# Optimization experiments

Hardware: AMD Instinct MI355X
Metric: run time of the kernel (lower is better)

Reference implementation:

```python
import jax, jax.numpy as jnp
import numpy as np


def setup_inputs() -> dict:
    key = jax.random.key(0)
    k1, k2, k3, k4, k5 = jax.random.split(key, 5)
    B, S, T = 512, 1024, 32
    emissions = jax.random.normal(k1, (B, S, T), dtype=jnp.float32)
    tags = jax.random.randint(k2, (B, S), 0, T, dtype=jnp.int64)
    mask = jnp.ones((B, S), dtype=jnp.float32)  # all positions valid; mask[:,0]==1 required
    transitions = jax.random.normal(k3, (T, T), dtype=jnp.float32)
    start_transitions = jax.random.normal(k4, (T,), dtype=jnp.float32)
    end_transitions = jax.random.normal(k5, (T,), dtype=jnp.float32)
    return {
        "emissions": emissions,
        "tags": tags,
        "mask": mask,
        "transitions": transitions,
        "start_transitions": start_transitions,
        "end_transitions": end_transitions,
    }


def _compute_score(emissions, tags, mask, transitions, start_transitions, end_transitions):
    # score of the gold path, fully vectorized over time
    # first step
    score = start_transitions[tags[:, 0]]
    score = score + jnp.take_along_axis(emissions[:, 0], tags[:, 0:1], axis=1)[:, 0]
    # steps 1..S-1
    emit = jnp.take_along_axis(emissions[:, 1:], tags[:, 1:, None], axis=2)[..., 0]  # [B,S-1]
    trans = transitions[tags[:, :-1], tags[:, 1:]]                                   # [B,S-1]
    score = score + ((emit + trans) * mask[:, 1:]).sum(axis=1)
    # end transition from the last valid tag
    last_idx = mask.sum(axis=1).astype(jnp.int32) - 1                                # [B]
    last_tags = jnp.take_along_axis(tags, last_idx[:, None].astype(tags.dtype), axis=1)[:, 0]
    score = score + end_transitions[last_tags]
    return score


def _compute_partition(emissions, mask, transitions, start_transitions, end_transitions):
    # forward algorithm: logsumexp scan over time
    alpha0 = start_transitions + emissions[:, 0]  # [B,T]

    def step(alpha, inp):
        e_i, m_i = inp  # e_i: [B,T], m_i: [B]
        # alpha[b,i] + transitions[i,j] + e_i[b,j] -> logsumexp over i
        scores = alpha[:, :, None] + transitions[None, :, :] + e_i[:, None, :]  # [B,T,T]
        next_alpha = jax.nn.logsumexp(scores, axis=1)                            # [B,T]
        m = m_i[:, None]
        alpha = next_alpha * m + alpha * (1.0 - m)
        return alpha, None

    xs = (jnp.swapaxes(emissions[:, 1:], 0, 1), jnp.swapaxes(mask[:, 1:], 0, 1))
    alpha, _ = jax.lax.scan(step, alpha0, xs)
    alpha = alpha + end_transitions
    return jax.nn.logsumexp(alpha, axis=1)  # [B]


def reference(emissions, tags, mask, transitions, start_transitions, end_transitions):
    score = _compute_score(emissions, tags, mask, transitions, start_transitions, end_transitions)
    partition = _compute_partition(emissions, mask, transitions, start_transitions, end_transitions)
    return -(score - partition).sum()
```

## Files before the change

kernel.cpp:

```cpp
#include <hip/hip_runtime.h>


typedef __attribute__((ext_vector_type(8)))  short    short8;
typedef __attribute__((ext_vector_type(16))) float    f32x16;
typedef __attribute__((ext_vector_type(4)))  unsigned uint4v;

#define S_N 1024
#define T_N 32
#define B_N 512
#define L_CH 64
#define C_CH 16
#define SCALE_MUL 0.0078125f
#define SCALE_LOG 4.852030263919617f

#define WS_FRAG_DW ((size_t)B_N * C_CH * 512)
#define WS_MSUM_OFF (WS_FRAG_DW)
#define WS_SCORE_OFF (WS_FRAG_DW + 512)
#define WS_NAPP_OFF (WS_FRAG_DW + 1024)

#if __has_builtin(__builtin_amdgcn_cvt_pk_bf16_f32)
typedef __attribute__((ext_vector_type(2))) __bf16 bf16x2;
__device__ __forceinline__ unsigned cvtpk(float lo, float hi) {
    return __builtin_bit_cast(unsigned, __builtin_amdgcn_cvt_pk_bf16_f32(lo, hi));
}
#else
__device__ __forceinline__ unsigned cvtpk(float lo, float hi) {
    const unsigned a = __float_as_uint(lo) + 0x8000u;
    const unsigned b = __float_as_uint(hi) + 0x8000u;
    return __builtin_amdgcn_perm(b, a, 0x07060302u);
}
#endif

__device__ __forceinline__ short8 mk8(const unsigned* a) {
    uint4v u = {a[0], a[1], a[2], a[3]};
    return __builtin_bit_cast(short8, u);
}
__device__ __forceinline__ float bflo(unsigned u) { return __uint_as_float(u << 16); }
__device__ __forceinline__ float bfhi(unsigned u) { return __uint_as_float(u & 0xFFFF0000u); }
__device__ __forceinline__ int PIx(int x) { return (x & ~12) | ((x & 4) << 1) | ((x & 8) >> 1); }

__global__ __launch_bounds__(256) void crf_chunk(
    const float* __restrict__ em, const int* __restrict__ tags,
    const float* __restrict__ mask, const float* __restrict__ trans,
    const float* __restrict__ startT, unsigned* __restrict__ wsf,
    float* __restrict__ wsflt)
{
    __shared__ unsigned elds[4][L_CH * 16];
    const int wib  = threadIdx.x >> 6;
    const int lane = threadIdx.x & 63;
    const int n    = lane & 31;
    const int h    = lane >> 5;
    const int wave = blockIdx.x * 4 + wib;
    const int b    = wave >> 4;
    const int c    = wave & (C_CH - 1);

    unsigned* my = elds[wib];
    const float* eb = em + ((size_t)b * S_N + c * L_CH) * T_N;

    #pragma unroll
    for (int i = 0; i < 16; ++i) {
        const int flat = i * 64 + lane;
        const int r = flat >> 4, m = flat & 15;
        const int base = ((m & 4) << 2) + ((m & 2) << 2) + ((m & 1) << 1) + ((m >> 3) << 2);
        const float2 v = *(const float2*)(eb + r * 32 + base);
        my[r * 16 + m] = cvtpk(__expf(v.x) * SCALE_MUL, __expf(v.y) * SCALE_MUL);
    }

    const int s0 = c * L_CH;
    const float mv_l = mask[b * S_N + s0 + lane];
    unsigned long long mbits = __ballot(mv_l != 0.0f);
    if (c == 0) mbits &= ~1ull;

    {
        const int s  = s0 + lane;
        const int tc = tags[b * S_N + s];
        int tp = __shfl_up(tc, 1, 64);
        float val;
        if (lane == 0) {
            if (c == 0) {
                val = startT[tc] + eb[tc];
            } else {
                tp = tags[b * S_N + s - 1];
                val = mv_l * (em[((size_t)b * S_N + s) * T_N + tc] + trans[tp * 32 + tc]);
            }
        } else {
            val = mv_l * (em[((size_t)b * S_N + s) * T_N + tc] + trans[tp * 32 + tc]);
        }
        float ms = mv_l;
        #pragma unroll
        for (int d = 32; d > 0; d >>= 1) {
            val += __shfl_xor(val, d, 64);
            ms  += __shfl_xor(ms,  d, 64);
        }
        if (lane == 0) {
            atomicAdd(&wsflt[WS_SCORE_OFF + b], val);
            atomicAdd(&wsflt[WS_MSUM_OFF + b], ms);
            wsflt[WS_NAPP_OFF + b * C_CH + c] = (float)__popcll(mbits);
        }
    }
    __syncthreads();

    const bool fwdDir = (c < 8);
    const f32x16 Zacc = {};

    unsigned A1[4], A2[4];
    #pragma unroll
    for (int j = 0; j < 4; ++j) {
        const int k1 = PIx(8 * h + 2 * j);
        const int k2 = PIx(16 + 8 * h + 2 * j);
        if (fwdDir) {
            A1[j] = cvtpk(__expf(trans[n * 32 + k1]), __expf(trans[n * 32 + k1 + 1]));
            A2[j] = cvtpk(__expf(trans[n * 32 + k2]), __expf(trans[n * 32 + k2 + 1]));
        } else {
            A1[j] = cvtpk(__expf(trans[k1 * 32 + n]), __expf(trans[(k1 + 1) * 32 + n]));
            A2[j] = cvtpk(__expf(trans[k2 * 32 + n]), __expf(trans[(k2 + 1) * 32 + n]));
        }
    }
    const short8 A1v = mk8(A1), A2v = mk8(A2);
    const bool clean = ((mbits | (c == 0 ? 1ull : 0ull)) == ~0ull);

    if (fwdDir) {
        f32x16 D;
        #pragma unroll
        for (int i = 0; i < 16; ++i) {
            const int row = (i & 3) + 8 * (i >> 2) + 4 * h;
            D[i] = (row == n) ? 1.0f : 0.0f;
        }
        #define STEP_FWD(r_) { \
            const uint4 su = *(const uint4*)(my + (r_) * 16 + h * 8); \
            const uint4 sv = *(const uint4*)(my + (r_) * 16 + h * 8 + 4); \
            unsigned S[8]; \
            S[0] = cvtpk(D[0]  * bflo(su.x), D[1]  * bfhi(su.x)); \
            S[1] = cvtpk(D[2]  * bflo(su.y), D[3]  * bfhi(su.y)); \
            S[2] = cvtpk(D[4]  * bflo(su.z), D[5]  * bfhi(su.z)); \
            S[3] = cvtpk(D[6]  * bflo(su.w), D[7]  * bfhi(su.w)); \
            S[4] = cvtpk(D[8]  * bflo(sv.x), D[9]  * bfhi(sv.x)); \
            S[5] = cvtpk(D[10] * bflo(sv.y), D[11] * bfhi(sv.y)); \
            S[6] = cvtpk(D[12] * bflo(sv.z), D[13] * bfhi(sv.z)); \
            S[7] = cvtpk(D[14] * bflo(sv.w), D[15] * bfhi(sv.w)); \
            f32x16 t_ = __builtin_amdgcn_mfma_f32_32x32x16_bf16(A1v, mk8(&S[0]), Zacc, 0, 0, 0); \
            D = __builtin_amdgcn_mfma_f32_32x32x16_bf16(A2v, mk8(&S[4]), t_, 0, 0, 0); \
        }
        if (clean) {
            #pragma unroll 4
            for (int r = 63; r >= 1; --r) STEP_FWD(r);
            if (c != 0) STEP_FWD(0);
        } else {
            for (int r = 63; r >= 0; --r)
                if ((mbits >> r) & 1ull) STEP_FWD(r);
        }
        unsigned* dst = wsf + ((size_t)(b * C_CH + c) * 64 + lane) * 8;
        ((uint4*)dst)[0] = make_uint4(cvtpk(D[0], D[1]),  cvtpk(D[2], D[3]),
                                      cvtpk(D[4], D[5]),  cvtpk(D[6], D[7]));
        ((uint4*)dst)[1] = make_uint4(cvtpk(D[8], D[9]),  cvtpk(D[10], D[11]),
                                      cvtpk(D[12], D[13]), cvtpk(D[14], D[15]));
    } else {
        unsigned S[8] = {0u, 0u, 0u, 0u, 0u, 0u, 0u, 0u};
        {
            const int pn = PIx(n);
            if (((pn >> 3) & 1) == h) {
                const int j = pn & 7;
                const unsigned val = 0x3F80u << (16 * (j & 1));
                if (n < 16) S[j >> 1] |= val; else S[4 + (j >> 1)] |= val;
            }
        }
        #define STEP_BWD(r_) { \
            f32x16 t_ = __builtin_amdgcn_mfma_f32_32x32x16_bf16(A1v, mk8(&S[0]), Zacc, 0, 0, 0); \
            t_ = __builtin_amdgcn_mfma_f32_32x32x16_bf16(A2v, mk8(&S[4]), t_, 0, 0, 0); \
            const uint4 su = *(const uint4*)(my + (r_) * 16 + h * 8); \
            const uint4 sv = *(const uint4*)(my + (r_) * 16 + h * 8 + 4); \
            S[0] = cvtpk(t_[0]  * bflo(su.x), t_[1]  * bfhi(su.x)); \
            S[1] = cvtpk(t_[2]  * bflo(su.y), t_[3]  * bfhi(su.y)); \
            S[2] = cvtpk(t_[4]  * bflo(su.z), t_[5]  * bfhi(su.z)); \
            S[3] = cvtpk(t_[6]  * bflo(su.w), t_[7]  * bfhi(su.w)); \
            S[4] = cvtpk(t_[8]  * bflo(sv.x), t_[9]  * bfhi(sv.x)); \
            S[5] = cvtpk(t_[10] * bflo(sv.y), t_[11] * bfhi(sv.y)); \
            S[6] = cvtpk(t_[12] * bflo(sv.z), t_[13] * bfhi(sv.z)); \
            S[7] = cvtpk(t_[14] * bflo(sv.w), t_[15] * bfhi(sv.w)); \
        }
        if (clean) {
            #pragma unroll 4
            for (int r = 0; r < 64; ++r) STEP_BWD(r);
        } else {
            for (int r = 0; r < 64; ++r)
                if ((mbits >> r) & 1ull) STEP_BWD(r);
        }
        unsigned* dst = wsf + ((size_t)(b * C_CH + c) * 64 + lane) * 8;
        ((uint4*)dst)[0] = make_uint4(S[0], S[1], S[2], S[3]);
        ((uint4*)dst)[1] = make_uint4(S[4], S[5], S[6], S[7]);
    }
}

__global__ __launch_bounds__(128) void crf_combine(
    const float* __restrict__ em, const int* __restrict__ tags,
    const float* __restrict__ startT, const float* __restrict__ endT,
    const unsigned* __restrict__ wsf, const float* __restrict__ wsflt,
    float* __restrict__ out)
{
    __shared__ float sm[68];
    const int lane = threadIdx.x & 63;
    const int w = threadIdx.x >> 6;
    const int n = lane & 31, h = lane >> 5;
    const int b = blockIdx.x;

    int idxA[8], idxB[8];
    #pragma unroll
    for (int j = 0; j < 8; ++j) {
        idxA[j] = PIx(8 * h + j);
        idxB[j] = PIx(16 + 8 * h + j);
    }

    float a0 = (w == 0) ? (startT[n] + em[(size_t)b * S_N * T_N + n]) : endT[n];
    float m = a0;
    #pragma unroll
    for (int d = 16; d > 0; d >>= 1) m = fmaxf(m, __shfl_xor(m, d, 32));
    float A = __expf(a0 - m);
    float Lacc = m;
    float ntot = 0.0f;

    const uint4* fb = (const uint4*)(wsf + (size_t)b * C_CH * 512);
    const int c0 = (w == 0) ? 0 : 15;
    const int dc = (w == 0) ? 1 : -1;
    uint4 q0 = fb[c0 * 128 + lane * 2];
    uint4 q1 = fb[c0 * 128 + lane * 2 + 1];

    for (int i = 0; i < 8; ++i) {
        const int c = c0 + i * dc;
        uint4 n0 = q0, n1 = q1;
        if (i + 1 < 8) {
            n0 = fb[(c + dc) * 128 + lane * 2];
            n1 = fb[(c + dc) * 128 + lane * 2 + 1];
        }
        ntot += wsflt[WS_NAPP_OFF + b * C_CH + c];

        float p0 = 0.f, p1 = 0.f, p2 = 0.f, p3 = 0.f;
        p0 = fmaf(__shfl(A, idxA[0], 32), bflo(q0.x), p0);
        p1 = fmaf(__shfl(A, idxA[1], 32), bfhi(q0.x), p1);
        p2 = fmaf(__shfl(A, idxA[2], 32), bflo(q0.y), p2);
        p3 = fmaf(__shfl(A, idxA[3], 32), bfhi(q0.y), p3);
        p0 = fmaf(__shfl(A, idxA[4], 32), bflo(q0.z), p0);
        p1 = fmaf(__shfl(A, idxA[5], 32), bfhi(q0.z), p1);
        p2 = fmaf(__shfl(A, idxA[6], 32), bflo(q0.w), p2);
        p3 = fmaf(__shfl(A, idxA[7], 32), bfhi(q0.w), p3);
        p0 = fmaf(__shfl(A, idxB[0], 32), bflo(q1.x), p0);
        p1 = fmaf(__shfl(A, idxB[1], 32), bfhi(q1.x), p1);
        p2 = fmaf(__shfl(A, idxB[2], 32), bflo(q1.y), p2);
        p3 = fmaf(__shfl(A, idxB[3], 32), bfhi(q1.y), p3);
        p0 = fmaf(__shfl(A, idxB[4], 32), bflo(q1.z), p0);
        p1 = fmaf(__shfl(A, idxB[5], 32), bfhi(q1.z), p1);
        p2 = fmaf(__shfl(A, idxB[6], 32), bflo(q1.w), p2);
        p3 = fmaf(__shfl(A, idxB[7], 32), bfhi(q1.w), p3);
        float part = (p0 + p1) + (p2 + p3);
        part += __shfl_xor(part, 32);

        float mm = part;
        #pragma unroll
        for (int d = 16; d > 0; d >>= 1) mm = fmaxf(mm, __shfl_xor(mm, d, 32));
        A = part / mm;
        Lacc += __logf(mm);
        q0 = n0; q1 = n1;
    }

    if (h == 0) sm[w * 32 + n] = A;
    if (lane == 0) { sm[64 + w] = Lacc; sm[66 + w] = ntot; }
    __syncthreads();

    if (threadIdx.x < 32) {
        float v = sm[threadIdx.x] * sm[32 + threadIdx.x];
        #pragma unroll
        for (int d = 16; d > 0; d >>= 1) v += __shfl_xor(v, d, 32);
        if (threadIdx.x == 0) {
            const float part = sm[64] + sm[65] + __logf(v) + (sm[66] + sm[67]) * SCALE_LOG;
            const int len = (int)(wsflt[WS_MSUM_OFF + b] + 0.5f);
            const int lt  = tags[b * S_N + len - 1];
            atomicAdd(out, part - endT[lt] - wsflt[WS_SCORE_OFF + b]);
        }
    }
}

extern "C" void kernel_launch(void* const* d_in, const int* in_sizes, int n_in,
                              void* d_out, int out_size, void* d_ws, size_t ws_size,
                              hipStream_t stream) {
    const float* em     = (const float*)d_in[0];
    const int*   tags   = (const int*)  d_in[1];
    const float* mask   = (const float*)d_in[2];
    const float* trans  = (const float*)d_in[3];
    const float* startT = (const float*)d_in[4];
    const float* endT   = (const float*)d_in[5];
    float* out = (float*)d_out;

    unsigned* wsf   = (unsigned*)d_ws;
    float*    wsflt = (float*)d_ws;

    hipMemsetAsync(out, 0, sizeof(float), stream);
    hipMemsetAsync((char*)d_ws + WS_MSUM_OFF * 4, 0, 4096, stream);

    hipLaunchKernelGGL(crf_chunk, dim3(2048), dim3(256), 0, stream,
                       em, tags, mask, trans, startT, wsf, wsflt);
    hipLaunchKernelGGL(crf_combine, dim3(512), dim3(128), 0, stream,
                       em, tags, startT, endT, wsf, wsflt, out);
}
```

Measured before the change: 178.3 us.

## Interleave four independent chunk chains per wave and drop backward direction

Each wave now processes four sequence chunks with interleaved MFMA recurrences, so the dependent matrix-product chains can hide each other's MFMA latency. All chunks use forward direction, which removes the backward path. Work per batch moves into one block with 64KB LDS, and the grid shrinks to 512 blocks. The combine kernel becomes one wave per batch doing all 16 chunks sequentially, with no shared-memory merge. Register pressure rises from the four accumulators, the grid is smaller, and the combine serial chain doubles in length.

```diff
diff --git a/kernel.cpp b/kernel.cpp
--- a/kernel.cpp
+++ b/kernel.cpp
@@ -39,169 +39,154 @@
 __device__ __forceinline__ float bfhi(unsigned u) { return __uint_as_float(u & 0xFFFF0000u); }
 __device__ __forceinline__ int PIx(int x) { return (x & ~12) | ((x & 4) << 1) | ((x & 8) >> 1); }
 
-__global__ __launch_bounds__(256) void crf_chunk(
+__global__ __launch_bounds__(256, 2) void crf_chunk(
     const float* __restrict__ em, const int* __restrict__ tags,
     const float* __restrict__ mask, const float* __restrict__ trans,
     const float* __restrict__ startT, unsigned* __restrict__ wsf,
     float* __restrict__ wsflt)
 {
-    __shared__ unsigned elds[4][L_CH * 16];
+    __shared__ unsigned elds[16384];
     const int wib  = threadIdx.x >> 6;
     const int lane = threadIdx.x & 63;
     const int n    = lane & 31;
     const int h    = lane >> 5;
-    const int wave = blockIdx.x * 4 + wib;
-    const int b    = wave >> 4;
-    const int c    = wave & (C_CH - 1);
-
-    unsigned* my = elds[wib];
-    const float* eb = em + ((size_t)b * S_N + c * L_CH) * T_N;
-
-    #pragma unroll
-    for (int i = 0; i < 16; ++i) {
-        const int flat = i * 64 + lane;
-        const int r = flat >> 4, m = flat & 15;
-        const int base = ((m & 4) << 2) + ((m & 2) << 2) + ((m & 1) << 1) + ((m >> 3) << 2);
-        const float2 v = *(const float2*)(eb + r * 32 + base);
-        my[r * 16 + m] = cvtpk(__expf(v.x) * SCALE_MUL, __expf(v.y) * SCALE_MUL);
-    }
-
-    const int s0 = c * L_CH;
-    const float mv_l = mask[b * S_N + s0 + lane];
-    unsigned long long mbits = __ballot(mv_l != 0.0f);
-    if (c == 0) mbits &= ~1ull;
-
+    const int b    = blockIdx.x;
+
+    #pragma unroll
+    for (int q = 0; q < 4; ++q) {
+        const float* eq = em + ((size_t)b * S_N + (4 * wib + q) * L_CH) * T_N;
+        unsigned* mq = elds + wib * 4096 + q * 1024;
+        #pragma unroll
+        for (int i = 0; i < 16; ++i) {
+            const int flat = i * 64 + lane;
+            const int r = flat >> 4, m = flat & 15;
+            const int base = ((m & 4) << 2) + ((m & 2) << 2) + ((m & 1) << 1) + ((m >> 3) << 2);
+            const float2 v = *(const float2*)(eq + r * 32 + base);
+            mq[r * 16 + m] = cvtpk(__expf(v.x) * SCALE_MUL, __expf(v.y) * SCALE_MUL);
+        }
+    }
+
+    unsigned long long mb_[4];
     {
-        const int s  = s0 + lane;
-        const int tc = tags[b * S_N + s];
-        int tp = __shfl_up(tc, 1, 64);
-        float val;
+        float vacc = 0.f, macc = 0.f;
+        #pragma unroll
+        for (int q = 0; q < 4; ++q) {
+            const int c = 4 * wib + q;
+            const int s = c * L_CH + lane;
+            const float mv = mask[b * S_N + s];
+            unsigned long long mb = __ballot(mv != 0.0f);
+            if (c == 0) mb &= ~1ull;
+            mb_[q] = mb;
+            const int tc = tags[b * S_N + s];
+            int tp = __shfl_up(tc, 1, 64);
+            float val;
+            if (lane == 0) {
+                if (c == 0) {
+                    val = startT[tc] + em[(size_t)b * S_N * T_N + tc];
+                } else {
+                    tp = tags[b * S_N + s - 1];
+                    val = mv * (em[((size_t)b * S_N + s) * T_N + tc] + trans[tp * 32 + tc]);
+                }
+            } else {
+                val = mv * (em[((size_t)b * S_N + s) * T_N + tc] + trans[tp * 32 + tc]);
+            }
+            vacc += val; macc += mv;
+            if (lane == 0) wsflt[WS_NAPP_OFF + b * C_CH + c] = (float)__popcll(mb);
+        }
+        #pragma unroll
+        for (int d = 32; d > 0; d >>= 1) {
+            vacc += __shfl_xor(vacc, d, 64);
+            macc += __shfl_xor(macc, d, 64);
+        }
         if (lane == 0) {
-            if (c == 0) {
-                val = startT[tc] + eb[tc];
-            } else {
-                tp = tags[b * S_N + s - 1];
-                val = mv_l * (em[((size_t)b * S_N + s) * T_N + tc] + trans[tp * 32 + tc]);
-            }
-        } else {
-            val = mv_l * (em[((size_t)b * S_N + s) * T_N + tc] + trans[tp * 32 + tc]);
-        }
-        float ms = mv_l;
-        #pragma unroll
-        for (int d = 32; d > 0; d >>= 1) {
-            val += __shfl_xor(val, d, 64);
-            ms  += __shfl_xor(ms,  d, 64);
-        }
-        if (lane == 0) {
-            atomicAdd(&wsflt[WS_SCORE_OFF + b], val);
-            atomicAdd(&wsflt[WS_MSUM_OFF + b], ms);
-            wsflt[WS_NAPP_OFF + b * C_CH + c] = (float)__popcll(mbits);
-        }
-    }
-    __syncthreads();
-
-    const bool fwdDir = (c < 8);
-    const f32x16 Zacc = {};
+            atomicAdd(&wsflt[WS_SCORE_OFF + b], vacc);
+            atomicAdd(&wsflt[WS_MSUM_OFF + b], macc);
+        }
+    }
 
     unsigned A1[4], A2[4];
     #pragma unroll
     for (int j = 0; j < 4; ++j) {
         const int k1 = PIx(8 * h + 2 * j);
         const int k2 = PIx(16 + 8 * h + 2 * j);
-        if (fwdDir) {
-            A1[j] = cvtpk(__expf(trans[n * 32 + k1]), __expf(trans[n * 32 + k1 + 1]));
-            A2[j] = cvtpk(__expf(trans[n * 32 + k2]), __expf(trans[n * 32 + k2 + 1]));
-        } else {
-            A1[j] = cvtpk(__expf(trans[k1 * 32 + n]), __expf(trans[(k1 + 1) * 32 + n]));
-            A2[j] = cvtpk(__expf(trans[k2 * 32 + n]), __expf(trans[(k2 + 1) * 32 + n]));
-        }
+        A1[j] = cvtpk(__expf(trans[n * 32 + k1]), __expf(trans[n * 32 + k1 + 1]));
+        A2[j] = cvtpk(__expf(trans[n * 32 + k2]), __expf(trans[n * 32 + k2 + 1]));
     }
     const short8 A1v = mk8(A1), A2v = mk8(A2);
-    const bool clean = ((mbits | (c == 0 ? 1ull : 0ull)) == ~0ull);
-
-    if (fwdDir) {
-        f32x16 D;
-        #pragma unroll
-        for (int i = 0; i < 16; ++i) {
-            const int row = (i & 3) + 8 * (i >> 2) + 4 * h;
-            D[i] = (row == n) ? 1.0f : 0.0f;
-        }
-        #define STEP_FWD(r_) { \
-            const uint4 su = *(const uint4*)(my + (r_) * 16 + h * 8); \
-            const uint4 sv = *(const uint4*)(my + (r_) * 16 + h * 8 + 4); \
-            unsigned S[8]; \
-            S[0] = cvtpk(D[0]  * bflo(su.x), D[1]  * bfhi(su.x)); \
-            S[1] = cvtpk(D[2]  * bflo(su.y), D[3]  * bfhi(su.y)); \
-            S[2] = cvtpk(D[4]  * bflo(su.z), D[5]  * bfhi(su.z)); \
-            S[3] = cvtpk(D[6]  * bflo(su.w), D[7]  * bfhi(su.w)); \
-            S[4] = cvtpk(D[8]  * bflo(sv.x), D[9]  * bfhi(sv.x)); \
-            S[5] = cvtpk(D[10] * bflo(sv.y), D[11] * bfhi(sv.y)); \
-            S[6] = cvtpk(D[12] * bflo(sv.z), D[13] * bfhi(sv.z)); \
-            S[7] = cvtpk(D[14] * bflo(sv.w), D[15] * bfhi(sv.w)); \
-            f32x16 t_ = __builtin_amdgcn_mfma_f32_32x32x16_bf16(A1v, mk8(&S[0]), Zacc, 0, 0, 0); \
-            D = __builtin_amdgcn_mfma_f32_32x32x16_bf16(A2v, mk8(&S[4]), t_, 0, 0, 0); \
-        }
-        if (clean) {
-            #pragma unroll 4
-            for (int r = 63; r >= 1; --r) STEP_FWD(r);
-            if (c != 0) STEP_FWD(0);
-        } else {
-            for (int r = 63; r >= 0; --r)
-                if ((mbits >> r) & 1ull) STEP_FWD(r);
-        }
-        unsigned* dst = wsf + ((size_t)(b * C_CH + c) * 64 + lane) * 8;
-        ((uint4*)dst)[0] = make_uint4(cvtpk(D[0], D[1]),  cvtpk(D[2], D[3]),
-                                      cvtpk(D[4], D[5]),  cvtpk(D[6], D[7]));
-        ((uint4*)dst)[1] = make_uint4(cvtpk(D[8], D[9]),  cvtpk(D[10], D[11]),
-                                      cvtpk(D[12], D[13]), cvtpk(D[14], D[15]));
+    const f32x16 Zacc = {};
+
+    f32x16 D0, D1, D2, D3;
+    #pragma unroll
+    for (int i = 0; i < 16; ++i) {
+        const int row = (i & 3) + 8 * (i >> 2) + 4 * h;
+        const float v = (row == n) ? 1.0f : 0.0f;
+        D0[i] = v; D1[i] = v; D2[i] = v; D3[i] = v;
+    }
+
+    const unsigned* m0 = elds + wib * 4096;
+    const unsigned* m1 = m0 + 1024;
+    const unsigned* m2 = m0 + 2048;
+    const unsigned* m3 = m0 + 3072;
+
+    #define STEP(D, mq, r_) { \
+        const uint4 su = *(const uint4*)((mq) + (r_) * 16 + h * 8); \
+        const uint4 sv = *(const uint4*)((mq) + (r_) * 16 + h * 8 + 4); \
+        unsigned S[8]; \
+        S[0] = cvtpk(D[0]  * bflo(su.x), D[1]  * bfhi(su.x)); \
+        S[1] = cvtpk(D[2]  * bflo(su.y), D[3]  * bfhi(su.y)); \
+        S[2] = cvtpk(D[4]  * bflo(su.z), D[5]  * bfhi(su.z)); \
+        S[3] = cvtpk(D[6]  * bflo(su.w), D[7]  * bfhi(su.w)); \
+        S[4] = cvtpk(D[8]  * bflo(sv.x), D[9]  * bfhi(sv.x)); \
+        S[5] = cvtpk(D[10] * bflo(sv.y), D[11] * bfhi(sv.y)); \
+        S[6] = cvtpk(D[12] * bflo(sv.z), D[13] * bfhi(sv.z)); \
+        S[7] = cvtpk(D[14] * bflo(sv.w), D[15] * bfhi(sv.w)); \
+        f32x16 t_ = __builtin_amdgcn_mfma_f32_32x32x16_bf16(A1v, mk8(&S[0]), Zacc, 0, 0, 0); \
+        D = __builtin_amdgcn_mfma_f32_32x32x16_bf16(A2v, mk8(&S[4]), t_, 0, 0, 0); \
+    }
+
+    const bool allclean =
+        ((mb_[0] | ((4 * wib) == 0 ? 1ull : 0ull)) == ~0ull) &&
+        (mb_[1] == ~0ull) && (mb_[2] == ~0ull) && (mb_[3] == ~0ull);
+
+    if (allclean) {
+        #pragma unroll 2
+        for (int r = L_CH - 1; r >= 1; --r) {
+            STEP(D0, m0, r); STEP(D1, m1, r); STEP(D2, m2, r); STEP(D3, m3, r);
+        }
+        if (mb_[0] & 1ull) STEP(D0, m0, 0);
+        if (mb_[1] & 1ull) STEP(D1, m1, 0);
+        if (mb_[2] & 1ull) STEP(D2, m2, 0);
+        if (mb_[3] & 1ull) STEP(D3, m3, 0);
     } else {
-        unsigned S[8] = {0u, 0u, 0u, 0u, 0u, 0u, 0u, 0u};
-        {
-            const int pn = PIx(n);
-            if (((pn >> 3) & 1) == h) {
-                const int j = pn & 7;
-                const unsigned val = 0x3F80u << (16 * (j & 1));
-                if (n < 16) S[j >> 1] |= val; else S[4 + (j >> 1)] |= val;
-            }
-        }
-        #define STEP_BWD(r_) { \
-            f32x16 t_ = __builtin_amdgcn_mfma_f32_32x32x16_bf16(A1v, mk8(&S[0]), Zacc, 0, 0, 0); \
-            t_ = __builtin_amdgcn_mfma_f32_32x32x16_bf16(A2v, mk8(&S[4]), t_, 0, 0, 0); \
-            const uint4 su = *(const uint4*)(my + (r_) * 16 + h * 8); \
-            const uint4 sv = *(const uint4*)(my + (r_) * 16 + h * 8 + 4); \
-            S[0] = cvtpk(t_[0]  * bflo(su.x), t_[1]  * bfhi(su.x)); \
-            S[1] = cvtpk(t_[2]  * bflo(su.y), t_[3]  * bfhi(su.y)); \
-            S[2] = cvtpk(t_[4]  * bflo(su.z), t_[5]  * bfhi(su.z)); \
-            S[3] = cvtpk(t_[6]  * bflo(su.w), t_[7]  * bfhi(su.w)); \
-            S[4] = cvtpk(t_[8]  * bflo(sv.x), t_[9]  * bfhi(sv.x)); \
-            S[5] = cvtpk(t_[10] * bflo(sv.y), t_[11] * bfhi(sv.y)); \
-            S[6] = cvtpk(t_[12] * bflo(sv.z), t_[13] * bfhi(sv.z)); \
-            S[7] = cvtpk(t_[14] * bflo(sv.w), t_[15] * bfhi(sv.w)); \
-        }
-        if (clean) {
-            #pragma unroll 4
-            for (int r = 0; r < 64; ++r) STEP_BWD(r);
-        } else {
-            for (int r = 0; r < 64; ++r)
-                if ((mbits >> r) & 1ull) STEP_BWD(r);
-        }
-        unsigned* dst = wsf + ((size_t)(b * C_CH + c) * 64 + lane) * 8;
-        ((uint4*)dst)[0] = make_uint4(S[0], S[1], S[2], S[3]);
-        ((uint4*)dst)[1] = make_uint4(S[4], S[5], S[6], S[7]);
-    }
-}
-
-__global__ __launch_bounds__(128) void crf_combine(
+        for (int r = L_CH - 1; r >= 0; --r) {
+            if ((mb_[0] >> r) & 1ull) STEP(D0, m0, r);
+            if ((mb_[1] >> r) & 1ull) STEP(D1, m1, r);
+            if ((mb_[2] >> r) & 1ull) STEP(D2, m2, r);
+            if ((mb_[3] >> r) & 1ull) STEP(D3, m3, r);
+        }
+    }
+    #undef STEP
+
+    #define STORE(D, q_) { \
+        unsigned* dst = wsf + ((size_t)(b * C_CH + 4 * wib + (q_)) * 64 + lane) * 8; \
+        ((uint4*)dst)[0] = make_uint4(cvtpk(D[0], D[1]),   cvtpk(D[2], D[3]), \
+                                      cvtpk(D[4], D[5]),   cvtpk(D[6], D[7])); \
+        ((uint4*)dst)[1] = make_uint4(cvtpk(D[8], D[9]),   cvtpk(D[10], D[11]), \
+                                      cvtpk(D[12], D[13]), cvtpk(D[14], D[15])); \
+    }
+    STORE(D0, 0) STORE(D1, 1) STORE(D2, 2) STORE(D3, 3)
+    #undef STORE
+}
+
+__global__ __launch_bounds__(256) void crf_combine(
     const float* __restrict__ em, const int* __restrict__ tags,
     const float* __restrict__ startT, const float* __restrict__ endT,
     const unsigned* __restrict__ wsf, const float* __restrict__ wsflt,
     float* __restrict__ out)
 {
-    __shared__ float sm[68];
     const int lane = threadIdx.x & 63;
-    const int w = threadIdx.x >> 6;
     const int n = lane & 31, h = lane >> 5;
-    const int b = blockIdx.x;
+    const int b = blockIdx.x * 4 + (threadIdx.x >> 6);
 
     int idxA[8], idxB[8];
     #pragma unroll
@@ -210,28 +195,24 @@
         idxB[j] = PIx(16 + 8 * h + j);
     }
 
-    float a0 = (w == 0) ? (startT[n] + em[(size_t)b * S_N * T_N + n]) : endT[n];
+    float a0 = startT[n] + em[(size_t)b * S_N * T_N + n];
     float m = a0;
     #pragma unroll
     for (int d = 16; d > 0; d >>= 1) m = fmaxf(m, __shfl_xor(m, d, 32));
     float A = __expf(a0 - m);
     float Lacc = m;
-    float ntot = 0.0f;
+    float ntot = (lane < 16) ? wsflt[WS_NAPP_OFF + b * C_CH + lane] : 0.0f;
 
     const uint4* fb = (const uint4*)(wsf + (size_t)b * C_CH * 512);
-    const int c0 = (w == 0) ? 0 : 15;
-    const int dc = (w == 0) ? 1 : -1;
-    uint4 q0 = fb[c0 * 128 + lane * 2];
-    uint4 q1 = fb[c0 * 128 + lane * 2 + 1];
-
-    for (int i = 0; i < 8; ++i) {
-        const int c = c0 + i * dc;
+    uint4 q0 = fb[lane * 2];
+    uint4 q1 = fb[lane * 2 + 1];
+
+    for (int c = 0; c < C_CH; ++c) {
         uint4 n0 = q0, n1 = q1;
-        if (i + 1 < 8) {
-            n0 = fb[(c + dc) * 128 + lane * 2];
-            n1 = fb[(c + dc) * 128 + lane * 2 + 1];
-        }
-        ntot += wsflt[WS_NAPP_OFF + b * C_CH + c];
+        if (c + 1 < C_CH) {
+            n0 = fb[(c + 1) * 128 + lane * 2];
+            n1 = fb[(c + 1) * 128 + lane * 2 + 1];
+        }
 
         float p0 = 0.f, p1 = 0.f, p2 = 0.f, p3 = 0.f;
         p0 = fmaf(__shfl(A, idxA[0], 32), bflo(q0.x), p0);
@@ -261,20 +242,18 @@
         q0 = n0; q1 = n1;
     }
 
-    if (h == 0) sm[w * 32 + n] = A;
-    if (lane == 0) { sm[64 + w] = Lacc; sm[66 + w] = ntot; }
-    __syncthreads();
-
-    if (threadIdx.x < 32) {
-        float v = sm[threadIdx.x] * sm[32 + threadIdx.x];
-        #pragma unroll
-        for (int d = 16; d > 0; d >>= 1) v += __shfl_xor(v, d, 32);
-        if (threadIdx.x == 0) {
-            const float part = sm[64] + sm[65] + __logf(v) + (sm[66] + sm[67]) * SCALE_LOG;
-            const int len = (int)(wsflt[WS_MSUM_OFF + b] + 0.5f);
-            const int lt  = tags[b * S_N + len - 1];
-            atomicAdd(out, part - endT[lt] - wsflt[WS_SCORE_OFF + b]);
-        }
+    float v = A * __expf(endT[n]);
+    #pragma unroll
+    for (int d = 16; d > 0; d >>= 1) {
+        v    += __shfl_xor(v, d, 32);
+        ntot += __shfl_xor(ntot, d, 32);
+    }
+    if (lane == 0) {
+        const int len = (int)(wsflt[WS_MSUM_OFF + b] + 0.5f);
+        const int lt  = tags[b * S_N + len - 1];
+        const float res = Lacc + __logf(v) + ntot * SCALE_LOG
+                          - endT[lt] - wsflt[WS_SCORE_OFF + b];
+        atomicAdd(out, res);
     }
 }
 
@@ -295,8 +274,8 @@
     hipMemsetAsync(out, 0, sizeof(float), stream);
     hipMemsetAsync((char*)d_ws + WS_MSUM_OFF * 4, 0, 4096, stream);
 
-    hipLaunchKernelGGL(crf_chunk, dim3(2048), dim3(256), 0, stream,
+    hipLaunchKernelGGL(crf_chunk, dim3(512), dim3(256), 0, stream,
                        em, tags, mask, trans, startT, wsf, wsflt);
-    hipLaunchKernelGGL(crf_combine, dim3(512), dim3(128), 0, stream,
+    hipLaunchKernelGGL(crf_combine, dim3(128), dim3(256), 0, stream,
                        em, tags, startT, endT, wsf, wsflt, out);
 }
```

New measurement: 173.2 us. -2.8%, faster.
